# Performance work log

Measured on AMD Instinct MI355X. Metric: run time of the kernel, lower is better.

The kernel has to match this reference:

```python
import jax, jax.numpy as jnp
import numpy as np

B, PQ, C, NH, L, P, FF = 8, 900, 256, 8, 4, 4, 2048
SHAPES = [(100, 152), (50, 76), (25, 38), (13, 19)]
PK = sum(h * w for h, w in SHAPES)
DH = C // NH


def setup_inputs() -> dict:
    key = jax.random.key(0)
    ks = jax.random.split(key, 20)
    s = 0.02
    w = lambda i, shp: jax.random.normal(ks[i], shp, jnp.float32) * s
    starts = np.cumsum([0] + [h * wd for h, wd in SHAPES[:-1]]).astype(np.int64)
    return dict(
        query=w(0, (B, C, PQ)),
        key=w(1, (B, C, PK)),
        query_pos=jax.random.uniform(ks[2], (B, PQ, 3)),
        key_pos=jax.random.uniform(ks[3], (B, PK, 3)),
        reference_points=jax.random.uniform(ks[4], (B, PQ, L, 2)),
        W_in=w(5, (3 * C, C)), b_in=jnp.zeros(3 * C),
        W_out=w(6, (C, C)), b_out=jnp.zeros(C),
        W_off=w(7, (NH * L * P * 2, C)),
        b_off=jax.random.uniform(ks[8], (NH * L * P * 2,), minval=-1.0, maxval=1.0),
        W_aw=w(9, (NH * L * P, C)), b_aw=jnp.zeros(NH * L * P),
        W_v=w(10, (C, C)), b_v=jnp.zeros(C),
        W_o=w(11, (C, C)), b_o=jnp.zeros(C),
        W1=w(12, (FF, C)), b1=jnp.zeros(FF),
        W2=w(13, (C, FF)), b2=jnp.zeros(C),
        g1=jnp.ones(C), be1=jnp.zeros(C),
        g2=jnp.ones(C), be2=jnp.zeros(C),
        g3=jnp.ones(C), be3=jnp.zeros(C),
        spatial_shapes=np.array(SHAPES, np.int64),
        level_start_index=starts,
    )


def layer_norm(x, g, b):
    m = x.mean(-1, keepdims=True)
    v = x.var(-1, keepdims=True)
    return (x - m) * jax.lax.rsqrt(v + 1e-5) * g + b


def mha(x, W_in, b_in, W_out, b_out):
    # x: [S, B, C]; torch nn.MultiheadAttention with q=k=v=x
    S, Bn, _ = x.shape
    qkv = x @ W_in.T + b_in
    q, k, v = jnp.split(qkv, 3, axis=-1)
    to_h = lambda t: t.reshape(S, Bn, NH, DH).transpose(1, 2, 0, 3)  # [B,H,S,Dh]
    q, k, v = to_h(q), to_h(k), to_h(v)
    attn = jax.nn.softmax(jnp.einsum('bhqd,bhkd->bhqk', q, k) / np.sqrt(DH), axis=-1)
    o = jnp.einsum('bhqk,bhkd->bhqd', attn, v).transpose(2, 0, 1, 3).reshape(S, Bn, C)
    return o @ W_out.T + b_out


def ms_deform(value, loc, aw, shapes, starts):
    # value [B,PK,NH,DH], loc [B,PQ,NH,L,P,2] in [0,1], aw [B,PQ,NH,L,P]
    v = value.transpose(0, 2, 1, 3)          # [B,NH,PK,DH]
    locT = loc.transpose(0, 2, 1, 3, 4, 5)   # [B,NH,PQ,L,P,2]
    awT = aw.transpose(0, 2, 1, 3, 4)        # [B,NH,PQ,L,P]
    out = jnp.zeros((B, NH, PQ, DH), value.dtype)
    for l, (Hl, Wl) in enumerate(shapes):
        st = starts[l]
        vl = v[:, :, st:st + Hl * Wl]        # [B,NH,Hl*Wl,DH]
        x = locT[..., l, :, 0] * Wl - 0.5    # [B,NH,PQ,P]  (align_corners=False)
        y = locT[..., l, :, 1] * Hl - 0.5
        x0 = jnp.floor(x); y0 = jnp.floor(y)
        lw, lh = x - x0, y - y0
        x0i = x0.astype(jnp.int32); y0i = y0.astype(jnp.int32)

        def gather(ix, iy):
            valid = ((ix >= 0) & (ix < Wl) & (iy >= 0) & (iy < Hl)).astype(vl.dtype)
            idx = jnp.clip(iy, 0, Hl - 1) * Wl + jnp.clip(ix, 0, Wl - 1)
            g = jnp.take_along_axis(vl, idx.reshape(B, NH, -1, 1), axis=2)
            return g.reshape(B, NH, PQ, P, DH) * valid[..., None]

        samp = (gather(x0i, y0i) * ((1 - lw) * (1 - lh))[..., None]
                + gather(x0i + 1, y0i) * (lw * (1 - lh))[..., None]
                + gather(x0i, y0i + 1) * ((1 - lw) * lh)[..., None]
                + gather(x0i + 1, y0i + 1) * (lw * lh)[..., None])  # [B,NH,PQ,P,DH]
        out = out + (samp * awT[..., l, :, None]).sum(3)
    return out.transpose(0, 2, 1, 3).reshape(B, PQ, C)


def reference(query, key, query_pos, key_pos, reference_points,
              W_in, b_in, W_out, b_out, W_off, b_off, W_aw, b_aw,
              W_v, b_v, W_o, b_o, W1, b1, W2, b2,
              g1, be1, g2, be2, g3, be3,
              spatial_shapes, level_start_index):
    shapes = [tuple(int(t) for t in r) for r in np.asarray(spatial_shapes)]
    starts = [int(t) for t in np.asarray(level_start_index)]
    q = query.transpose(2, 0, 1)   # [PQ,B,C]
    k = key.transpose(2, 0, 1)     # [PK,B,C]
    # self-attention (posembeds are None in this config)
    q = layer_norm(q + mha(q, W_in, b_in, W_out, b_out), g1, be1)
    # multi-scale deformable cross-attention
    qd = q.transpose(1, 0, 2)      # [B,PQ,C]
    kf = k.transpose(1, 0, 2)      # [B,PK,C]
    value = (kf @ W_v.T + b_v).reshape(B, PK, NH, DH)
    off = (qd @ W_off.T + b_off).reshape(B, PQ, NH, L, P, 2)
    aw = jax.nn.softmax((qd @ W_aw.T + b_aw).reshape(B, PQ, NH, L * P), -1)
    aw = aw.reshape(B, PQ, NH, L, P)
    norm = jnp.asarray([[w_, h_] for (h_, w_) in shapes], jnp.float32)  # [L,2] as (W,H)
    loc = reference_points[:, :, None, :, None, :] + off / norm[None, None, None, :, None, :]
    q2 = ms_deform(value, loc, aw, shapes, starts) @ W_o.T + b_o
    q = layer_norm(q + q2.transpose(1, 0, 2), g2, be2)
    # FFN
    ff = jax.nn.relu(q @ W1.T + b1) @ W2.T + b2
    q = layer_norm(q + ff, g3, be3)
    return q.transpose(1, 2, 0)    # [B,C,PQ]
```

## Files before the change

### kernel.cpp

```cpp
#include <hip/hip_runtime.h>
#include <hip/hip_bf16.h>
#include <stdint.h>

typedef __hip_bfloat16 bf16;
typedef short bf16x8 __attribute__((ext_vector_type(8)));
typedef short s4v    __attribute__((ext_vector_type(4)));
typedef float f32x4  __attribute__((ext_vector_type(4)));

constexpr int B_  = 8;
constexpr int PQ_ = 900;
constexpr int C_  = 256;
constexpr int NH_ = 8;
constexpr int L_  = 4;
constexpr int P_  = 4;
constexpr int FF_ = 2048;
constexpr int DH_ = 32;
constexpr int PK_ = 20197;
constexpr int VLD = 960;
constexpr int64_t FFS = (int64_t)B_ * PQ_ * C_;

__device__ __forceinline__ short f2b(float f) {
    __hip_bfloat16 h = __float2bfloat16(f);
    union { __hip_bfloat16 h; short s; } u; u.h = h; return u.s;
}
__device__ __forceinline__ float b2f(short s) {
    union { short s; __hip_bfloat16 h; } u; u.s = s; return __bfloat162float(u.h);
}

__launch_bounds__(256)
__global__ void wcvt_kernel(const float* __restrict__ p0, const float* __restrict__ p1,
                            const float* __restrict__ p2, const float* __restrict__ p3,
                            const float* __restrict__ p4, const float* __restrict__ p5,
                            const float* __restrict__ p6, const float* __restrict__ p7,
                            short* __restrict__ dst)
{
    const int g = (blockIdx.x * 256 + threadIdx.x) * 4;
    const float* src; int off;
    if      (g < 196608)  { src = p0; off = 0; }
    else if (g < 262144)  { src = p1; off = 196608; }
    else if (g < 327680)  { src = p2; off = 262144; }
    else if (g < 360448)  { src = p3; off = 327680; }
    else if (g < 425984)  { src = p4; off = 360448; }
    else if (g < 491520)  { src = p5; off = 425984; }
    else if (g < 1015808) { src = p6; off = 491520; }
    else                  { src = p7; off = 1015808; }
    float4 v = *(const float4*)(src + (g - off));
    s4v pk = {f2b(v.x), f2b(v.y), f2b(v.z), f2b(v.w)};
    *(s4v*)&dst[g] = pk;
}

__launch_bounds__(512)
__global__ void vgemm3_kernel(const float* __restrict__ key, const short* __restrict__ Wv,
                              const float* __restrict__ bias, short* __restrict__ value,
                              int Mb)
{
    constexpr int CST = 40;
    __shared__ short Sh[8 * 64 * CST];
    short* As = Sh;

    const int tid = threadIdx.x;
    const int wv = tid >> 6, lane = tid & 63;
    const int quad = lane >> 4, lrow = lane & 15;

    const int m0 = blockIdx.x * 64;
    const int gm = m0 + lane;
    const bool va = gm < Mb;
    int b = 0, s = 0;
    if (va) { b = gm / PK_; s = gm - b * PK_; }
    const int64_t rbase = (int64_t)(b * 256) * PK_ + s;

#pragma unroll
    for (int jj = 0; jj < 4; ++jj) {
        short pk[8];
#pragma unroll
        for (int j = 0; j < 8; ++j) {
            const int c = wv * 32 + jj * 8 + j;
            pk[j] = f2b(va ? key[rbase + (int64_t)c * PK_] : 0.f);
        }
        const int slot = wv * 4 + jj;
        const int phys = (slot + lane) & 31;
        *(bf16x8*)&As[lane * 256 + phys * 8] = *(const bf16x8*)pk;
    }
    __syncthreads();

    float bia[2];
#pragma unroll
    for (int nf = 0; nf < 2; ++nf) bia[nf] = bias[wv * 32 + nf * 16 + lrow];

    f32x4 acc[4][2];
#pragma unroll
    for (int mf = 0; mf < 4; ++mf)
#pragma unroll
        for (int nf = 0; nf < 2; ++nf) acc[mf][nf] = (f32x4){0.f, 0.f, 0.f, 0.f};

#pragma unroll
    for (int kh = 0; kh < 8; ++kh) {
        bf16x8 a[4];
#pragma unroll
        for (int mf = 0; mf < 4; ++mf) {
            const int r = mf * 16 + lrow;
            const int phys = ((kh * 4 + quad) + r) & 31;
            a[mf] = *(const bf16x8*)&As[r * 256 + phys * 8];
        }
        bf16x8 wf[2];
#pragma unroll
        for (int nf = 0; nf < 2; ++nf)
            wf[nf] = *(const bf16x8*)&Wv[(int64_t)(wv * 32 + nf * 16 + lrow) * 256 + kh * 32 + quad * 8];
#pragma unroll
        for (int mf = 0; mf < 4; ++mf)
#pragma unroll
            for (int nf = 0; nf < 2; ++nf)
                acc[mf][nf] = __builtin_amdgcn_mfma_f32_16x16x32_bf16(a[mf], wf[nf], acc[mf][nf], 0, 0, 0);
    }
    __syncthreads();

    short* Cs = &Sh[wv * 64 * CST];
#pragma unroll
    for (int nf = 0; nf < 2; ++nf)
#pragma unroll
        for (int mf = 0; mf < 4; ++mf)
#pragma unroll
            for (int r = 0; r < 4; ++r)
                Cs[(mf * 16 + quad * 4 + r) * CST + nf * 16 + lrow] = f2b(acc[mf][nf][r] + bia[nf]);
#pragma unroll
    for (int jj = 0; jj < 4; ++jj) {
        const int row = (lane >> 2) + jj * 16;
        const int rr = m0 + row;
        bf16x8 pk = *(const bf16x8*)&Cs[row * CST + (lane & 3) * 8];
        if (rr < Mb)
            *(bf16x8*)&value[(int64_t)rr * 256 + wv * 32 + (lane & 3) * 8] = pk;
    }
}

template <int NF, int MF, bool DBUF, bool AF32, bool WF32, bool CF32, bool RELU>
__launch_bounds__(256)
__global__ void mfma_gemm(const void* __restrict__ Ap, const void* __restrict__ Wp,
                          const float* __restrict__ bias, void* __restrict__ Cp,
                          int Mb, int N, int K, int tilesM,
                          int ldA, int ldW, int ldC, int nbI,
                          int64_t sAo, int64_t sAi, int64_t sWo, int64_t sWi,
                          int64_t sCo, int64_t sCi, float scale,
                          const float* __restrict__ bias2, int nsplit)
{
    constexpr int BM  = MF * 16;
    constexpr int BN  = 64 * NF;
    constexpr int LDR = 72;
    constexpr int NB  = DBUF ? 2 : 1;
    constexpr int TPR = 256 / BM;
    constexpr int SPT = 64 / TPR;
    constexpr int CHA = SPT / 8;
    __shared__ short As[NB * BM * LDR];
    __shared__ short Ws[NB * BN * LDR];

    const int tid   = threadIdx.x;
    const int batch = blockIdx.y / tilesM;
    const int m0    = (blockIdx.y % tilesM) * BM;
    const int n0    = blockIdx.x * BN;
    const int outer = batch / nbI, inner = batch % nbI;
    const int64_t offA = (int64_t)outer * sAo + (int64_t)inner * sAi;
    const int64_t offW = (int64_t)outer * sWo + (int64_t)inner * sWi;
    const int64_t offC = (int64_t)outer * sCo + (int64_t)inner * sCi;

    const int w = tid >> 6, lane = tid & 63;
    const int quad = lane >> 4, lrow = lane & 15;
    const int colbase = n0 + w * 16 * NF;

    const int smA = tid / TPR;
    const int skA = (tid % TPR) * SPT;
    const int smW = tid >> 2;
    const int skW = (tid & 3) * 16;

    const int T = (K + 63) / 64;

    bf16x8 areg[CHA];
    bf16x8 wreg[2 * NF];

    auto stageA = [&](int t) {
        const int k0 = t * 64;
        const int gm = m0 + smA;
#pragma unroll
        for (int c = 0; c < CHA; ++c) {
            const int k = k0 + skA + c * 8;
            bf16x8 pk = {0, 0, 0, 0, 0, 0, 0, 0};
            if (gm < Mb && k + 8 <= K) {
                if (AF32) {
                    const float* s = (const float*)Ap + offA + (int64_t)gm * ldA + k;
                    float4 u0 = *(const float4*)s;
                    float4 u1 = *(const float4*)(s + 4);
                    pk = (bf16x8){f2b(u0.x), f2b(u0.y), f2b(u0.z), f2b(u0.w),
                                  f2b(u1.x), f2b(u1.y), f2b(u1.z), f2b(u1.w)};
                } else {
                    pk = *(const bf16x8*)((const short*)Ap + offA + (int64_t)gm * ldA + k);
                }
            }
            areg[c] = pk;
        }
    };
    auto stageW = [&](int t) {
        const int k0 = t * 64;
#pragma unroll
        for (int j = 0; j < NF; ++j) {
            const int gn = n0 + j * 64 + smW;
#pragma unroll
            for (int c = 0; c < 2; ++c) {
                const int k = k0 + skW + c * 8;
                bf16x8 pk = {0, 0, 0, 0, 0, 0, 0, 0};
                if (gn < N && k + 8 <= K) {
                    if (WF32) {
                        const float* s = (const float*)Wp + offW + (int64_t)gn * ldW + k;
                        float4 u0 = *(const float4*)s;
                        float4 u1 = *(const float4*)(s + 4);
                        pk = (bf16x8){f2b(u0.x), f2b(u0.y), f2b(u0.z), f2b(u0.w),
                                      f2b(u1.x), f2b(u1.y), f2b(u1.z), f2b(u1.w)};
                    } else {
                        pk = *(const bf16x8*)((const short*)Wp + offW + (int64_t)gn * ldW + k);
                    }
                }
                wreg[j * 2 + c] = pk;
            }
        }
    };
    auto writeLDS = [&](int buf) {
#pragma unroll
        for (int c = 0; c < CHA; ++c)
            *(bf16x8*)&As[(buf * BM + smA) * LDR + skA + c * 8] = areg[c];
#pragma unroll
        for (int j = 0; j < NF; ++j)
#pragma unroll
            for (int c = 0; c < 2; ++c)
                *(bf16x8*)&Ws[(buf * BN + j * 64 + smW) * LDR + skW + c * 8] = wreg[j * 2 + c];
    };

    f32x4 acc[MF][NF];
#pragma unroll
    for (int i = 0; i < MF; ++i)
#pragma unroll
        for (int j = 0; j < NF; ++j) acc[i][j] = (f32x4){0.f, 0.f, 0.f, 0.f};

    auto compute = [&](int buf) {
        bf16x8 a[MF][2], bb[NF][2];
#pragma unroll
        for (int kh = 0; kh < 2; ++kh) {
#pragma unroll
            for (int mf = 0; mf < MF; ++mf)
                a[mf][kh] = *(const bf16x8*)&As[(buf * BM + mf * 16 + lrow) * LDR + kh * 32 + quad * 8];
#pragma unroll
            for (int nf = 0; nf < NF; ++nf)
                bb[nf][kh] = *(const bf16x8*)&Ws[(buf * BN + w * 16 * NF + nf * 16 + lrow) * LDR + kh * 32 + quad * 8];
        }
#pragma unroll
        for (int kh = 0; kh < 2; ++kh)
#pragma unroll
            for (int mf = 0; mf < MF; ++mf)
#pragma unroll
                for (int nf = 0; nf < NF; ++nf)
                    acc[mf][nf] = __builtin_amdgcn_mfma_f32_16x16x32_bf16(a[mf][kh], bb[nf][kh], acc[mf][nf], 0, 0, 0);
    };

    if (DBUF) {
        stageA(0); stageW(0); writeLDS(0);
        __syncthreads();
        for (int t = 0; t < T; ++t) {
            const int cur = t & 1;
            if (t + 1 < T) { stageA(t + 1); stageW(t + 1); }
            compute(cur);
            if (t + 1 < T) {
                writeLDS(cur ^ 1);
                __syncthreads();
            }
        }
    } else {
        for (int t = 0; t < T; ++t) {
            stageA(t); stageW(t);
            if (t > 0) __syncthreads();
            writeLDS(0);
            __syncthreads();
            compute(0);
        }
    }

#pragma unroll
    for (int nf = 0; nf < NF; ++nf) {
        const int col = colbase + nf * 16 + lrow;
        if (col >= N) continue;
        float bia;
        if (col < nsplit) bia = bias ? bias[col] : 0.f;
        else              bia = bias2[col - nsplit];
#pragma unroll
        for (int mf = 0; mf < MF; ++mf) {
            const int row0 = m0 + mf * 16 + quad * 4;
#pragma unroll
            for (int r = 0; r < 4; ++r) {
                const int rr = row0 + r;
                if (rr < Mb) {
                    float v = acc[mf][nf][r] * scale + bia;
                    if (RELU) v = fmaxf(v, 0.f);
                    const int64_t idx = offC + (int64_t)rr * ldC + col;
                    if (CF32) ((float*)Cp)[idx] = v;
                    else      ((short*)Cp)[idx] = f2b(v);
                }
            }
        }
    }
}

template <int NF, int MF, bool DBUF, bool AF32, bool WF32, bool CF32, bool RELU>
static void mfma_launch(const void* A, const void* W, const float* bias, void* Cp,
                        int nb, int nbI, int Mb, int N, int K,
                        int ldA, int ldW, int ldC,
                        int64_t sAo, int64_t sAi, int64_t sWo, int64_t sWi,
                        int64_t sCo, int64_t sCi, float scale, hipStream_t stream,
                        const float* bias2 = nullptr, int nsplit = 1 << 30)
{
    constexpr int BM = MF * 16;
    int tilesM = (Mb + BM - 1) / BM;
    dim3 grid((N + 64 * NF - 1) / (64 * NF), nb * tilesM);
    mfma_gemm<NF, MF, DBUF, AF32, WF32, CF32, RELU><<<grid, 256, 0, stream>>>(
        A, W, bias, Cp, Mb, N, K, tilesM, ldA, ldW, ldC, nbI,
        sAo, sAi, sWo, sWi, sCo, sCi, scale, bias2, nsplit);
}

__launch_bounds__(256)
__global__ void transpose_kernel(const float* __restrict__ src, short* __restrict__ dst,
                                 int Scount, int ldS, int64_t sbs, int64_t dbs)
{
    const int tid = threadIdx.x;
    const int b = blockIdx.z;
    const int s0 = blockIdx.x * 32, c0 = blockIdx.y * 32;
    __shared__ float t[32][33];
    {
        const int c_l = tid >> 3, sq = (tid & 7) * 4;
        const int64_t base = (int64_t)b * sbs + (int64_t)(c0 + c_l) * ldS;
#pragma unroll
        for (int i = 0; i < 4; ++i) {
            const int s = s0 + sq + i;
            t[c_l][sq + i] = (s < Scount) ? src[base + s] : 0.f;
        }
    }
    __syncthreads();
    {
        const int s_l = tid >> 3, cq = (tid & 7) * 4;
        const int s = s0 + s_l;
        if (s < Scount) {
            s4v pk = {f2b(t[cq + 0][s_l]), f2b(t[cq + 1][s_l]),
                      f2b(t[cq + 2][s_l]), f2b(t[cq + 3][s_l])};
            *(s4v*)&dst[(int64_t)b * dbs + (int64_t)s * 256 + c0 + cq] = pk;
        }
    }
}

__launch_bounds__(256)
__global__ void vt_kernel(const short* __restrict__ qkv, short* __restrict__ VT)
{
    const int tid = threadIdx.x;
    const int bh = blockIdx.y, b = bh >> 3, h = bh & 7;
    const int s0 = blockIdx.x * 32;
    __shared__ short t[32][36];
    {
        const int s_l = tid >> 3, dq = (tid & 7) * 4;
        const int s = s0 + s_l;
        s4v pk = {0, 0, 0, 0};
        if (s < 900)
            pk = *(const s4v*)&qkv[((int64_t)(b * 900 + s)) * 768 + 512 + h * 32 + dq];
        *(s4v*)&t[s_l][dq] = pk;
    }
    __syncthreads();
    {
        const int d = tid >> 3, sq = (tid & 7) * 4;
        s4v pk = {t[sq + 0][d], t[sq + 1][d], t[sq + 2][d], t[sq + 3][d]};
        *(s4v*)&VT[((int64_t)bh * 32 + d) * VLD + s0 + sq] = pk;
    }
}

__launch_bounds__(256)
__global__ void attn_fused(const short* __restrict__ qkv, const short* __restrict__ VT,
                           short* __restrict__ attno)
{
    __shared__ short Pl[4 * 16 * 72];
    const int tid = threadIdx.x;
    const int wv = tid >> 6, lane = tid & 63;
    const int quad = lane >> 4, lrow = lane & 15;
    const int bh = blockIdx.y, b = bh >> 3, h = bh & 7;
    const int q0 = blockIdx.x * 64 + wv * 16;
    const float iscale = 0.17677669529663687f;

    bf16x8 aq = {0, 0, 0, 0, 0, 0, 0, 0};
    {
        const int q = q0 + lrow;
        if (q < 900)
            aq = *(const bf16x8*)&qkv[((int64_t)(b * 900 + q)) * 768 + h * 32 + quad * 8];
    }

    float lsum[4];
    f32x4 o[2] = {{0.f, 0.f, 0.f, 0.f}, {0.f, 0.f, 0.f, 0.f}};
#pragma unroll
    for (int r = 0; r < 4; ++r) lsum[r] = 0.f;

    short* Pw = &Pl[wv * 16 * 72];

    for (int st = 0; st < 15; ++st) {
        const int s0 = st * 64;
        f32x4 sc[4];
#pragma unroll
        for (int nf = 0; nf < 4; ++nf) {
            const int s = s0 + nf * 16 + lrow;
            bf16x8 kb = {0, 0, 0, 0, 0, 0, 0, 0};
            if (s < 900)
                kb = *(const bf16x8*)&qkv[((int64_t)(b * 900 + s)) * 768 + 256 + h * 32 + quad * 8];
            sc[nf] = __builtin_amdgcn_mfma_f32_16x16x32_bf16(aq, kb, (f32x4){0.f, 0.f, 0.f, 0.f}, 0, 0, 0);
        }
#pragma unroll
        for (int nf = 0; nf < 4; ++nf) {
            const int s = s0 + nf * 16 + lrow;
            if (s >= 900) sc[nf] = (f32x4){-1e30f, -1e30f, -1e30f, -1e30f};
            else {
#pragma unroll
                for (int r = 0; r < 4; ++r) sc[nf][r] *= iscale;
            }
        }
        float ps[4][4];
#pragma unroll
        for (int r = 0; r < 4; ++r) {
            float s4 = 0.f;
#pragma unroll
            for (int nf = 0; nf < 4; ++nf) {
                const float p = __expf(sc[nf][r]);
                ps[nf][r] = p;
                s4 += p;
            }
#pragma unroll
            for (int off = 1; off < 16; off <<= 1)
                s4 += __shfl_xor(s4, off, 64);
            lsum[r] += s4;
        }
#pragma unroll
        for (int nf = 0; nf < 4; ++nf)
#pragma unroll
            for (int r = 0; r < 4; ++r)
                Pw[(quad * 4 + r) * 72 + nf * 16 + lrow] = f2b(ps[nf][r]);
#pragma unroll
        for (int kh = 0; kh < 2; ++kh) {
            bf16x8 pa = *(const bf16x8*)&Pw[lrow * 72 + kh * 32 + quad * 8];
#pragma unroll
            for (int nf2 = 0; nf2 < 2; ++nf2) {
                const int d = nf2 * 16 + lrow;
                bf16x8 vb = *(const bf16x8*)&VT[((int64_t)bh * 32 + d) * VLD + s0 + kh * 32 + quad * 8];
                o[nf2] = __builtin_amdgcn_mfma_f32_16x16x32_bf16(pa, vb, o[nf2], 0, 0, 0);
            }
        }
    }
#pragma unroll
    for (int r = 0; r < 4; ++r) {
        const int q = q0 + quad * 4 + r;
        if (q < 900) {
            const float inv = 1.f / lsum[r];
#pragma unroll
            for (int nf2 = 0; nf2 < 2; ++nf2)
                attno[((int64_t)(b * 900 + q)) * 256 + h * 32 + nf2 * 16 + lrow] = f2b(o[nf2][r] * inv);
        }
    }
}

template <int MODE>
__launch_bounds__(256)
__global__ void ln_kernel(const float* __restrict__ y, const void* __restrict__ res,
                          const float* __restrict__ g, const float* __restrict__ be,
                          float* __restrict__ out_f, short* __restrict__ out_b,
                          const float* __restrict__ eb)
{
    const int bt = blockIdx.x;
    const int b = bt / PQ_, t = bt % PQ_;
    const int c = threadIdx.x;
    const int wv = c >> 6, lane = c & 63;

    float r;
    if (MODE == 0)      r = ((const float*)res)[((int64_t)b * C_ + c) * PQ_ + t];
    else if (MODE == 1) r = ((const float*)res)[(int64_t)bt * C_ + c];
    else                r = b2f(((const short*)res)[(int64_t)bt * C_ + c]);

    float yv;
    if (MODE == 2) {
        yv = eb[c];
#pragma unroll
        for (int i = 0; i < 4; ++i)
            yv += y[(int64_t)i * FFS + (int64_t)bt * C_ + c];
    } else {
        yv = y[(int64_t)bt * C_ + c];
    }
    const float v = r + yv;

    __shared__ float p1[4], p2[4];
    float a = v, sq = v * v;
#pragma unroll
    for (int off = 32; off > 0; off >>= 1) {
        a  += __shfl_xor(a, off, 64);
        sq += __shfl_xor(sq, off, 64);
    }
    if (lane == 0) { p1[wv] = a; p2[wv] = sq; }
    __syncthreads();
    const float s1 = p1[0] + p1[1] + p1[2] + p1[3];
    const float s2 = p2[0] + p2[1] + p2[2] + p2[3];
    const float mean = s1 * (1.f / C_);
    const float var  = s2 * (1.f / C_) - mean * mean;
    const float o = (v - mean) * rsqrtf(var + 1e-5f) * g[c] + be[c];

    if (MODE == 0) { out_f[(int64_t)bt * C_ + c] = o; out_b[(int64_t)bt * C_ + c] = f2b(o); }
    else if (MODE == 1) out_b[(int64_t)bt * C_ + c] = f2b(o);
    else out_f[((int64_t)b * C_ + c) * PQ_ + t] = o;
}

__launch_bounds__(512)
__global__ void deform_kernel(const float* __restrict__ oa,
                              const float* __restrict__ refp, const short* __restrict__ value,
                              short* __restrict__ samp)
{
    const int tid = threadIdx.x;
    const int lph = tid >> 8;
    const int q   = (tid >> 7) & 1;
    const int h   = (tid >> 4) & 7;
    const int dp  = tid & 15;
    const int bt  = blockIdx.x * 2 + q;
    const int b   = bt / PQ_;

    __shared__ float Loff[2][256];
    __shared__ float Law[2][128];
    __shared__ float Lref[2][8];
    __shared__ float Red[2][8][16][2];

    Loff[tid >> 8][tid & 255] = oa[(int64_t)(blockIdx.x * 2 + (tid >> 8)) * 384 + (tid & 255)];
    if (tid < 256)
        Law[tid >> 7][tid & 127] = oa[(int64_t)(blockIdx.x * 2 + (tid >> 7)) * 384 + 256 + (tid & 127)];
    if (tid < 16)
        Lref[tid >> 3][tid & 7] = refp[(int64_t)(blockIdx.x * 2 + (tid >> 3)) * 8 + (tid & 7)];
    __syncthreads();

    float m = -1e30f;
#pragma unroll
    for (int i = 0; i < 16; ++i) m = fmaxf(m, Law[q][h * 16 + i]);
    float s = 0.f;
#pragma unroll
    for (int i = 0; i < 16; ++i) s += __expf(Law[q][h * 16 + i] - m);
    const float invs = 1.f / s;

    float acc0 = 0.f, acc1 = 0.f;
#pragma unroll
    for (int li = 0; li < 2; ++li) {
        const int l   = 2 * lph + li;
        const int Hl  = (lph == 0) ? (li == 0 ? 100 : 50)   : (li == 0 ? 25 : 13);
        const int Wl  = (lph == 0) ? (li == 0 ? 152 : 76)   : (li == 0 ? 38 : 19);
        const int st0 = (lph == 0) ? (li == 0 ? 0 : 15200)  : (li == 0 ? 19000 : 19950);
        const float fx = Lref[q][l * 2 + 0], fy = Lref[q][l * 2 + 1];
#pragma unroll
        for (int p = 0; p < P_; ++p) {
            const float ox = Loff[q][h * 32 + l * 8 + p * 2 + 0];
            const float oy = Loff[q][h * 32 + l * 8 + p * 2 + 1];
            const float x = (fx + ox / (float)Wl) * (float)Wl - 0.5f;
            const float y = (fy + oy / (float)Hl) * (float)Hl - 0.5f;
            const float x0f = floorf(x), y0f = floorf(y);
            const int x0 = (int)x0f, y0 = (int)y0f;
            const float lw = x - x0f, lh = y - y0f;
            const float w00 = (1.f - lw) * (1.f - lh), w10 = lw * (1.f - lh);
            const float w01 = (1.f - lw) * lh,         w11 = lw * lh;
            const float aww = __expf(Law[q][h * 16 + l * 4 + p] - m) * invs;

            float sv0 = 0.f, sv1 = 0.f;
            int ix, iy; float w;
#pragma unroll
            for (int cidx = 0; cidx < 4; ++cidx) {
                if (cidx == 0) { ix = x0;     iy = y0;     w = w00; }
                if (cidx == 1) { ix = x0 + 1; iy = y0;     w = w10; }
                if (cidx == 2) { ix = x0;     iy = y0 + 1; w = w01; }
                if (cidx == 3) { ix = x0 + 1; iy = y0 + 1; w = w11; }
                if (ix >= 0 && ix < Wl && iy >= 0 && iy < Hl) {
                    const int64_t vi = ((int64_t)(b * PK_ + st0 + iy * Wl + ix)) * 256 + h * 32 + dp * 2;
                    const uint32_t pr = *(const uint32_t*)&value[vi];
                    sv0 += w * b2f((short)(pr & 0xffff));
                    sv1 += w * b2f((short)(pr >> 16));
                }
            }
            acc0 += sv0 * aww;
            acc1 += sv1 * aww;
        }
    }

    if (lph == 1) { Red[q][h][dp][0] = acc0; Red[q][h][dp][1] = acc1; }
    __syncthreads();
    if (lph == 0) {
        acc0 += Red[q][h][dp][0];
        acc1 += Red[q][h][dp][1];
        union { uint32_t u; short s2[2]; } o;
        o.s2[0] = f2b(acc0);
        o.s2[1] = f2b(acc1);
        *(uint32_t*)&samp[(int64_t)bt * 256 + h * 32 + dp * 2] = o.u;
    }
}

extern "C" void kernel_launch(void* const* d_in, const int* in_sizes, int n_in,
                              void* d_out, int out_size, void* d_ws, size_t ws_size,
                              hipStream_t stream)
{
    const float* query = (const float*)d_in[0];
    const float* key   = (const float*)d_in[1];
    const float* refp  = (const float*)d_in[4];
    const float* W_in  = (const float*)d_in[5];
    const float* b_in  = (const float*)d_in[6];
    const float* W_out = (const float*)d_in[7];
    const float* b_out = (const float*)d_in[8];
    const float* W_off = (const float*)d_in[9];
    const float* b_off = (const float*)d_in[10];
    const float* W_aw  = (const float*)d_in[11];
    const float* b_aw  = (const float*)d_in[12];
    const float* W_v   = (const float*)d_in[13];
    const float* b_v   = (const float*)d_in[14];
    const float* W_o   = (const float*)d_in[15];
    const float* b_o   = (const float*)d_in[16];
    const float* W1    = (const float*)d_in[17];
    const float* b1    = (const float*)d_in[18];
    const float* W2    = (const float*)d_in[19];
    const float* b2    = (const float*)d_in[20];
    const float* g1    = (const float*)d_in[21];
    const float* be1   = (const float*)d_in[22];
    const float* g2    = (const float*)d_in[23];
    const float* be2   = (const float*)d_in[24];
    const float* g3    = (const float*)d_in[25];
    const float* be3   = (const float*)d_in[26];

    char* X  = (char*)d_ws;
    char* Yb = X + 62259200;
    char* Z1 = Yb + 7372800;
    char* Wa = Z1 + 7372800;
    char* Wb_ = Wa + 3686400;
    char* VA = Wb_ + 3686400;
    char* WB = VA + 82726912;
    char* OA = WB + 3080192;
    char* FFP = OA + 11059200;

    short* qkvb   = (short*)X;
    short* queryT = (short*)(X + 11059200);
    short* VT     = (short*)(X + 14745600);
    short* attno  = (short*)(X + 18677760);
    short* ffh    = (short*)X;
    float* proj   = (float*)Yb;
    float* q1     = (float*)Z1;
    short* q1b    = (short*)Wa;
    short* samp   = (short*)Wa;
    short* q2nb   = (short*)Wb_;
    short* value  = (short*)VA;
    float* oa     = (float*)OA;
    float* ffp    = (float*)FFP;

    short* WBs    = (short*)WB;
    short* Wb_in  = WBs;
    short* Wb_out = WBs + 196608;
    short* Wb_off = WBs + 262144;
    short* Wb_v   = WBs + 360448;
    short* Wb_o   = WBs + 425984;
    short* Wb1    = WBs + 491520;
    short* Wb2    = WBs + 1015808;

    wcvt_kernel<<<1504, 256, 0, stream>>>(W_in, W_out, W_off, W_aw, W_v, W_o, W1, W2, WBs);
    transpose_kernel<<<dim3(29, 8, B_), 256, 0, stream>>>(query, queryT, PQ_, PQ_,
                                                          (int64_t)C_ * PQ_, (int64_t)PQ_ * C_);
    mfma_launch<1, 4, true, false, false, false, false>(queryT, Wb_in, b_in, qkvb, 1, 1, B_ * PQ_, 768, 256,
                                                        256, 256, 768, 0, 0, 0, 0, 0, 0, 1.f, stream);
    vt_kernel<<<dim3(30, 64), 256, 0, stream>>>(qkvb, VT);
    attn_fused<<<dim3(15, 64), 256, 0, stream>>>(qkvb, VT, attno);
    mfma_launch<1, 2, true, false, false, true, false>(attno, Wb_out, b_out, proj, 1, 1, B_ * PQ_, 256, 256,
                                                       256, 256, 256, 0, 0, 0, 0, 0, 0, 1.f, stream);
    ln_kernel<0><<<B_ * PQ_, 256, 0, stream>>>(proj, query, g1, be1, q1, q1b, nullptr);
    mfma_launch<1, 2, true, false, false, true, false>(q1b, Wb_off, b_off, oa, 1, 1, B_ * PQ_, 384, 256,
                                                       256, 256, 384, 0, 0, 0, 0, 0, 0, 1.f, stream,
                                                       b_aw, 256);
    vgemm3_kernel<<<(B_ * PK_ + 63) / 64, 512, 0, stream>>>(key, Wb_v, b_v, value, B_ * PK_);
    deform_kernel<<<B_ * PQ_ / 2, 512, 0, stream>>>(oa, refp, value, samp);
    mfma_launch<1, 2, true, false, false, true, false>(samp, Wb_o, b_o, proj, 1, 1, B_ * PQ_, 256, 256,
                                                       256, 256, 256, 0, 0, 0, 0, 0, 0, 1.f, stream);
    ln_kernel<1><<<B_ * PQ_, 256, 0, stream>>>(proj, q1, g2, be2, nullptr, q2nb, nullptr);
    mfma_launch<1, 4, true, false, false, false, true>(q2nb, Wb1, b1, ffh, 1, 1, B_ * PQ_, FF_, 256,
                                                       256, 256, FF_, 0, 0, 0, 0, 0, 0, 1.f, stream);
    mfma_launch<1, 4, true, false, false, true, false>(ffh, Wb2, nullptr, ffp, 4, 1, B_ * PQ_, 256, 512,
                                                       FF_, FF_, 256,
                                                       512, 0, 512, 0, FFS, 0, 1.f, stream);
    ln_kernel<2><<<B_ * PQ_, 256, 0, stream>>>(ffp, q2nb, g3, be3, (float*)d_out, nullptr, b2);

    (void)in_sizes; (void)n_in; (void)out_size; (void)ws_size;
}
```

Before: 627.4 us.

## Fuse query transpose into QKV GEMM and batch four rows per LN0 block

Removes the separate transpose kernel and folds the fp32-to-bf16 transpose of query into a new QKV projection kernel. That kernel loads the [B,C,PQ] input straight into LDS with a swizzled layout and runs MFMA against the bf16 in-proj weights. The first layer norm now handles four tokens per block, so it can read the channel-major residual with float4 loads instead of strided scalar loads. The trade-off is that the fused kernel's global reads are strided per channel, and it re-reads the whole A tile for each of the three N-blocks.

```diff
diff --git a/kernel.cpp b/kernel.cpp
--- a/kernel.cpp
+++ b/kernel.cpp
@@ -129,6 +129,90 @@
         bf16x8 pk = *(const bf16x8*)&Cs[row * CST + (lane & 3) * 8];
         if (rr < Mb)
             *(bf16x8*)&value[(int64_t)rr * 256 + wv * 32 + (lane & 3) * 8] = pk;
+    }
+}
+
+__launch_bounds__(512)
+__global__ void qkvt_kernel(const float* __restrict__ query, const short* __restrict__ Wq,
+                            const float* __restrict__ bias, short* __restrict__ qkv,
+                            int Mb)
+{
+    constexpr int CST = 40;
+    __shared__ short Sh[8 * 64 * CST];
+    short* As = Sh;
+
+    const int tid = threadIdx.x;
+    const int wv = tid >> 6, lane = tid & 63;
+    const int quad = lane >> 4, lrow = lane & 15;
+
+    const int m0 = blockIdx.x * 64;
+    const int n0 = blockIdx.y * 256;
+    const int gm = m0 + lane;
+    const bool va = gm < Mb;
+    int b = 0, t = 0;
+    if (va) { b = gm / PQ_; t = gm - b * PQ_; }
+    const int64_t rbase = (int64_t)(b * 256) * PQ_ + t;
+
+#pragma unroll
+    for (int jj = 0; jj < 4; ++jj) {
+        short pk[8];
+#pragma unroll
+        for (int j = 0; j < 8; ++j) {
+            const int c = wv * 32 + jj * 8 + j;
+            pk[j] = f2b(va ? query[rbase + (int64_t)c * PQ_] : 0.f);
+        }
+        const int slot = wv * 4 + jj;
+        const int phys = (slot + lane) & 31;
+        *(bf16x8*)&As[lane * 256 + phys * 8] = *(const bf16x8*)pk;
+    }
+    __syncthreads();
+
+    float bia[2];
+#pragma unroll
+    for (int nf = 0; nf < 2; ++nf) bia[nf] = bias[n0 + wv * 32 + nf * 16 + lrow];
+
+    f32x4 acc[4][2];
+#pragma unroll
+    for (int mf = 0; mf < 4; ++mf)
+#pragma unroll
+        for (int nf = 0; nf < 2; ++nf) acc[mf][nf] = (f32x4){0.f, 0.f, 0.f, 0.f};
+
+#pragma unroll
+    for (int kh = 0; kh < 8; ++kh) {
+        bf16x8 a[4];
+#pragma unroll
+        for (int mf = 0; mf < 4; ++mf) {
+            const int r = mf * 16 + lrow;
+            const int phys = ((kh * 4 + quad) + r) & 31;
+            a[mf] = *(const bf16x8*)&As[r * 256 + phys * 8];
+        }
+        bf16x8 wf[2];
+#pragma unroll
+        for (int nf = 0; nf < 2; ++nf)
+            wf[nf] = *(const bf16x8*)&Wq[(int64_t)(n0 + wv * 32 + nf * 16 + lrow) * 256 + kh * 32 + quad * 8];
+#pragma unroll
+        for (int mf = 0; mf < 4; ++mf)
+#pragma unroll
+            for (int nf = 0; nf < 2; ++nf)
+                acc[mf][nf] = __builtin_amdgcn_mfma_f32_16x16x32_bf16(a[mf], wf[nf], acc[mf][nf], 0, 0, 0);
+    }
+    __syncthreads();
+
+    short* Cs = &Sh[wv * 64 * CST];
+#pragma unroll
+    for (int nf = 0; nf < 2; ++nf)
+#pragma unroll
+        for (int mf = 0; mf < 4; ++mf)
+#pragma unroll
+            for (int r = 0; r < 4; ++r)
+                Cs[(mf * 16 + quad * 4 + r) * CST + nf * 16 + lrow] = f2b(acc[mf][nf][r] + bia[nf]);
+#pragma unroll
+    for (int jj = 0; jj < 4; ++jj) {
+        const int row = (lane >> 2) + jj * 16;
+        const int rr = m0 + row;
+        bf16x8 pk = *(const bf16x8*)&Cs[row * CST + (lane & 3) * 8];
+        if (rr < Mb)
+            *(bf16x8*)&qkv[(int64_t)rr * 768 + n0 + wv * 32 + (lane & 3) * 8] = pk;
     }
 }
 
@@ -321,35 +405,6 @@
 }
 
 __launch_bounds__(256)
-__global__ void transpose_kernel(const float* __restrict__ src, short* __restrict__ dst,
-                                 int Scount, int ldS, int64_t sbs, int64_t dbs)
-{
-    const int tid = threadIdx.x;
-    const int b = blockIdx.z;
-    const int s0 = blockIdx.x * 32, c0 = blockIdx.y * 32;
-    __shared__ float t[32][33];
-    {
-        const int c_l = tid >> 3, sq = (tid & 7) * 4;
-        const int64_t base = (int64_t)b * sbs + (int64_t)(c0 + c_l) * ldS;
-#pragma unroll
-        for (int i = 0; i < 4; ++i) {
-            const int s = s0 + sq + i;
-            t[c_l][sq + i] = (s < Scount) ? src[base + s] : 0.f;
-        }
-    }
-    __syncthreads();
-    {
-        const int s_l = tid >> 3, cq = (tid & 7) * 4;
-        const int s = s0 + s_l;
-        if (s < Scount) {
-            s4v pk = {f2b(t[cq + 0][s_l]), f2b(t[cq + 1][s_l]),
-                      f2b(t[cq + 2][s_l]), f2b(t[cq + 3][s_l])};
-            *(s4v*)&dst[(int64_t)b * dbs + (int64_t)s * 256 + c0 + cq] = pk;
-        }
-    }
-}
-
-__launch_bounds__(256)
 __global__ void vt_kernel(const short* __restrict__ qkv, short* __restrict__ VT)
 {
     const int tid = threadIdx.x;
@@ -461,6 +516,53 @@
     }
 }
 
+__launch_bounds__(256)
+__global__ void ln0_kernel(const float* __restrict__ y, const float* __restrict__ query,
+                           const float* __restrict__ g, const float* __restrict__ be,
+                           float* __restrict__ out_f, short* __restrict__ out_b)
+{
+    const int bt0 = blockIdx.x * 4;
+    const int b = bt0 / PQ_;
+    const int t0 = bt0 - b * PQ_;
+    const int c = threadIdx.x;
+    const int wv = c >> 6, lane = c & 63;
+
+    const float4 r4 = *(const float4*)&query[((int64_t)(b * C_ + c)) * PQ_ + t0];
+    float v[4];
+    v[0] = r4.x; v[1] = r4.y; v[2] = r4.z; v[3] = r4.w;
+#pragma unroll
+    for (int i = 0; i < 4; ++i)
+        v[i] += y[(int64_t)(bt0 + i) * C_ + c];
+
+    float sa[4], sb[4];
+#pragma unroll
+    for (int i = 0; i < 4; ++i) { sa[i] = v[i]; sb[i] = v[i] * v[i]; }
+#pragma unroll
+    for (int off = 32; off > 0; off >>= 1) {
+#pragma unroll
+        for (int i = 0; i < 4; ++i) {
+            sa[i] += __shfl_xor(sa[i], off, 64);
+            sb[i] += __shfl_xor(sb[i], off, 64);
+        }
+    }
+    __shared__ float p1[4][4], p2[4][4];
+    if (lane == 0) {
+#pragma unroll
+        for (int i = 0; i < 4; ++i) { p1[wv][i] = sa[i]; p2[wv][i] = sb[i]; }
+    }
+    __syncthreads();
+#pragma unroll
+    for (int i = 0; i < 4; ++i) {
+        const float s1 = p1[0][i] + p1[1][i] + p1[2][i] + p1[3][i];
+        const float s2 = p2[0][i] + p2[1][i] + p2[2][i] + p2[3][i];
+        const float mean = s1 * (1.f / C_);
+        const float var  = s2 * (1.f / C_) - mean * mean;
+        const float o = (v[i] - mean) * rsqrtf(var + 1e-5f) * g[c] + be[c];
+        out_f[(int64_t)(bt0 + i) * C_ + c] = o;
+        out_b[(int64_t)(bt0 + i) * C_ + c] = f2b(o);
+    }
+}
+
 template <int MODE>
 __launch_bounds__(256)
 __global__ void ln_kernel(const float* __restrict__ y, const void* __restrict__ res,
@@ -474,9 +576,8 @@
     const int wv = c >> 6, lane = c & 63;
 
     float r;
-    if (MODE == 0)      r = ((const float*)res)[((int64_t)b * C_ + c) * PQ_ + t];
-    else if (MODE == 1) r = ((const float*)res)[(int64_t)bt * C_ + c];
-    else                r = b2f(((const short*)res)[(int64_t)bt * C_ + c]);
+    if (MODE == 1) r = ((const float*)res)[(int64_t)bt * C_ + c];
+    else           r = b2f(((const short*)res)[(int64_t)bt * C_ + c]);
 
     float yv;
     if (MODE == 2) {
@@ -504,8 +605,7 @@
     const float var  = s2 * (1.f / C_) - mean * mean;
     const float o = (v - mean) * rsqrtf(var + 1e-5f) * g[c] + be[c];
 
-    if (MODE == 0) { out_f[(int64_t)bt * C_ + c] = o; out_b[(int64_t)bt * C_ + c] = f2b(o); }
-    else if (MODE == 1) out_b[(int64_t)bt * C_ + c] = f2b(o);
+    if (MODE == 1) out_b[(int64_t)bt * C_ + c] = f2b(o);
     else out_f[((int64_t)b * C_ + c) * PQ_ + t] = o;
 }
 
@@ -636,7 +736,6 @@
     char* FFP = OA + 11059200;
 
     short* qkvb   = (short*)X;
-    short* queryT = (short*)(X + 11059200);
     short* VT     = (short*)(X + 14745600);
     short* attno  = (short*)(X + 18677760);
     short* ffh    = (short*)X;
@@ -659,15 +758,12 @@
     short* Wb2    = WBs + 1015808;
 
     wcvt_kernel<<<1504, 256, 0, stream>>>(W_in, W_out, W_off, W_aw, W_v, W_o, W1, W2, WBs);
-    transpose_kernel<<<dim3(29, 8, B_), 256, 0, stream>>>(query, queryT, PQ_, PQ_,
-                                                          (int64_t)C_ * PQ_, (int64_t)PQ_ * C_);
-    mfma_launch<1, 4, true, false, false, false, false>(queryT, Wb_in, b_in, qkvb, 1, 1, B_ * PQ_, 768, 256,
-                                                        256, 256, 768, 0, 0, 0, 0, 0, 0, 1.f, stream);
+    qkvt_kernel<<<dim3(113, 3), 512, 0, stream>>>(query, Wb_in, b_in, qkvb, B_ * PQ_);
     vt_kernel<<<dim3(30, 64), 256, 0, stream>>>(qkvb, VT);
     attn_fused<<<dim3(15, 64), 256, 0, stream>>>(qkvb, VT, attno);
     mfma_launch<1, 2, true, false, false, true, false>(attno, Wb_out, b_out, proj, 1, 1, B_ * PQ_, 256, 256,
                                                        256, 256, 256, 0, 0, 0, 0, 0, 0, 1.f, stream);
-    ln_kernel<0><<<B_ * PQ_, 256, 0, stream>>>(proj, query, g1, be1, q1, q1b, nullptr);
+    ln0_kernel<<<B_ * PQ_ / 4, 256, 0, stream>>>(proj, query, g1, be1, q1, q1b);
     mfma_launch<1, 2, true, false, false, true, false>(q1b, Wb_off, b_off, oa, 1, 1, B_ * PQ_, 384, 256,
                                                        256, 256, 384, 0, 0, 0, 0, 0, 0, 1.f, stream,
                                                        b_aw, 256);
```

Measured after the change: 632.5 us. About the same (+0.8%).
